# Optimization experiments

Hardware: AMD Instinct MI355X
Metric: run time of the kernel (lower is better)

Reference implementation:

```python
import jax, jax.numpy as jnp
import numpy as np

N_NODES = 100000
N_EDGES = 600000
D = 128
N_CLASSES = 16


def _degrees(idx, n):
    ones = jnp.ones(idx.shape[0], dtype=jnp.float32)
    return jax.ops.segment_sum(ones, idx, num_segments=n)


def graph_conv(src, dst, h, W, b):
    # DGL GraphConv, norm='both': D_out^{-1/2} A D_in^{-1/2} h W + b
    n = h.shape[0]
    deg_out = jnp.maximum(_degrees(src, n), 1.0)
    deg_in = jnp.maximum(_degrees(dst, n), 1.0)
    h = h * jax.lax.rsqrt(deg_out)[:, None]          # src-side norm
    h = h @ W                                         # dense transform
    msg = h[src]                                      # gather  [E, d]
    agg = jax.ops.segment_sum(msg, dst, num_segments=n)  # scatter-add
    agg = agg * jax.lax.rsqrt(deg_in)[:, None]        # dst-side norm
    return agg + b


def setup_inputs() -> dict:
    key = jax.random.key(0)
    ks = jax.random.split(key, 8)
    h = jax.random.normal(ks[0], (N_NODES, D), dtype=jnp.float32)
    src = jax.random.randint(ks[1], (N_EDGES,), 0, N_NODES)
    dst = jax.random.randint(ks[2], (N_EDGES,), 0, N_NODES)
    s = 1.0 / np.sqrt(D)
    W1 = jax.random.normal(ks[3], (D, D), dtype=jnp.float32) * s
    b1 = jnp.zeros((D,), dtype=jnp.float32)
    W2 = jax.random.normal(ks[4], (D, D), dtype=jnp.float32) * s
    b2 = jnp.zeros((D,), dtype=jnp.float32)
    Wc = jax.random.normal(ks[5], (D, N_CLASSES), dtype=jnp.float32) * s
    bc = jnp.zeros((N_CLASSES,), dtype=jnp.float32)
    return {"h": h, "src": src, "dst": dst, "W1": W1, "b1": b1,
            "W2": W2, "b2": b2, "Wc": Wc, "bc": bc}


def reference(h, src, dst, W1, b1, W2, b2, Wc, bc):
    h = jax.nn.relu(graph_conv(src, dst, h, W1, b1))
    h = jax.nn.relu(graph_conv(src, dst, h, W2, b2))
    return h @ Wc + bc
```

## Files before the change

kernel.cpp:

```cpp
#include <hip/hip_runtime.h>


typedef __attribute__((ext_vector_type(4))) _Float16 half4_t;
typedef __attribute__((ext_vector_type(16))) float floatx16;

__global__ __launch_bounds__(256) void scan1_kernel(
    const int* __restrict__ cntI, const int* __restrict__ cntO,
    int* __restrict__ excl, int* __restrict__ bsum,
    float* __restrict__ rs_out, float* __restrict__ rs_in, int n)
{
    __shared__ int tmp[256];
    int i = blockIdx.x * 256 + threadIdx.x;
    int v = 0;
    if (i < n) {
        v = cntI[i];
        rs_in[i]  = rsqrtf(fmaxf((float)v, 1.0f));
        rs_out[i] = rsqrtf(fmaxf((float)cntO[i], 1.0f));
    }
    tmp[threadIdx.x] = v;
    __syncthreads();
    for (int off = 1; off < 256; off <<= 1) {
        int t = (threadIdx.x >= off) ? tmp[threadIdx.x - off] : 0;
        __syncthreads();
        tmp[threadIdx.x] += t;
        __syncthreads();
    }
    if (i < n) excl[i] = tmp[threadIdx.x] - v;
    if (threadIdx.x == 255) bsum[blockIdx.x] = tmp[255];
}

__global__ __launch_bounds__(1024) void scan2_kernel(int* __restrict__ bsum, int nb)
{
    __shared__ int tmp[1024];
    int t = threadIdx.x;
    int v = (t < nb) ? bsum[t] : 0;
    tmp[t] = v;
    __syncthreads();
    for (int off = 1; off < 1024; off <<= 1) {
        int x = (t >= off) ? tmp[t - off] : 0;
        __syncthreads();
        tmp[t] += x;
        __syncthreads();
    }
    if (t < nb) bsum[t] = tmp[t] - v;
}

__global__ __launch_bounds__(256) void scan3_kernel(
    int* __restrict__ excl, const int* __restrict__ bsum, int n)
{
    int i = blockIdx.x * 256 + threadIdx.x;
    if (i < n) excl[i] += bsum[blockIdx.x];
}

__global__ __launch_bounds__(256) void fill_kernel(
    const int* __restrict__ src, const int* __restrict__ dst,
    const int* __restrict__ rank, const int* __restrict__ starts,
    int* __restrict__ eidx, int E)
{
    int e = blockIdx.x * blockDim.x + threadIdx.x;
    if (e < E) {
        eidx[starts[dst[e]] + rank[e]] = src[e];
    }
}

__global__ __launch_bounds__(256) void wpack_kernel(
    const float* __restrict__ W1, const float* __restrict__ W2,
    _Float16* __restrict__ WB1, _Float16* __restrict__ WB2)
{
    int gid = blockIdx.x * 256 + threadIdx.x;
    int j = gid & 16383;
    int i   = j & 3;
    int col = (j >> 2) & 127;
    int g   = (j >> 9) & 1;
    int kt  = j >> 10;
    int k = kt * 8 + g * 4 + i;
    if (gid < 16384) WB1[j] = (_Float16)W1[k * 128 + col];
    else             WB2[j] = (_Float16)W2[k * 128 + col];
}

template <int MODE>
__device__ __forceinline__ void gemm_tile(
    int bid, const void* __restrict__ Xv, const _Float16* __restrict__ WB,
    _Float16* __restrict__ T, int n)
{
    __shared__ _Float16 xa[128 * 128];
    char* xab = (char*)xa;

    const int tid  = threadIdx.x;
    const int lane = tid & 63;
    const int wv   = tid >> 6;
    const int m    = lane & 31;
    const int g    = lane >> 5;
    const int rbase = bid * 128 + wv * 32;

    {
        const int C = (tid & 31) * 4;
        const int rsub = tid >> 5;
#pragma unroll
        for (int p = 0; p < 16; ++p) {
            int R = p * 8 + rsub;
            int row = bid * 128 + R;
            half4_t a;
            if (row < n) {
                if (MODE == 0) {
                    const float* X = (const float*)Xv;
                    float4 v = *(const float4*)&X[(size_t)row * 128 + C];
                    a[0] = (_Float16)v.x;
                    a[1] = (_Float16)v.y;
                    a[2] = (_Float16)v.z;
                    a[3] = (_Float16)v.w;
                } else {
                    const _Float16* X = (const _Float16*)Xv;
                    a = *(const half4_t*)&X[(size_t)row * 128 + C];
                }
            } else {
                a[0] = a[1] = a[2] = a[3] = (_Float16)0.f;
            }
            int byte = (R * 256 + C * 2) ^ ((R & 7) << 4);
            *(half4_t*)(xab + byte) = a;
        }
    }
    __syncthreads();

    floatx16 acc0 = {}, acc1 = {}, acc2 = {}, acc3 = {};
    const int arow = wv * 32 + m;
    const _Float16* wb = WB + (size_t)(g * 128 + m) * 4;

#pragma unroll 2
    for (int kt = 0; kt < 16; ++kt) {
        int cbyte = kt * 16 + g * 8;
        half4_t a = *(const half4_t*)(xab + ((arow * 256 + cbyte) ^ ((m & 7) << 4)));
        const _Float16* wk = wb + (size_t)kt * 1024;
        half4_t b0 = *(const half4_t*)(wk);
        half4_t b1 = *(const half4_t*)(wk + 128);
        half4_t b2 = *(const half4_t*)(wk + 256);
        half4_t b3 = *(const half4_t*)(wk + 384);
        acc0 = __builtin_amdgcn_mfma_f32_32x32x8f16(a, b0, acc0, 0, 0, 0);
        acc1 = __builtin_amdgcn_mfma_f32_32x32x8f16(a, b1, acc1, 0, 0, 0);
        acc2 = __builtin_amdgcn_mfma_f32_32x32x8f16(a, b2, acc2, 0, 0, 0);
        acc3 = __builtin_amdgcn_mfma_f32_32x32x8f16(a, b3, acc3, 0, 0, 0);
    }

#pragma unroll
    for (int rg = 0; rg < 16; ++rg) {
        int rd = (rg & 3) + 8 * (rg >> 2) + 4 * g;
        int orow = rbase + rd;
        if (orow < n) {
            _Float16* tp = T + (size_t)orow * 128 + m;
            tp[0]  = (_Float16)acc0[rg];
            tp[32] = (_Float16)acc1[rg];
            tp[64] = (_Float16)acc2[rg];
            tp[96] = (_Float16)acc3[rg];
        }
    }
}

__global__ __launch_bounds__(256) void fused1_kernel(
    const float* __restrict__ h, const _Float16* __restrict__ WB1,
    _Float16* __restrict__ T1,
    const int* __restrict__ src, const int* __restrict__ dst,
    int* __restrict__ cntO, int* __restrict__ cntI, int* __restrict__ rank,
    int n, int E, int GB, int S)
{
    int bid = blockIdx.x;
    int g = bid / S, r = bid - g * S;
    if (r == 0 && g < GB) {
        gemm_tile<0>(g, h, WB1, T1, n);
    } else {
        int ng = g + (r ? 1 : 0);
        if (ng > GB) ng = GB;
        int cb = bid - ng;
        int t = cb * 256 + threadIdx.x;
        if (t < E) {
            atomicAdd(&cntO[src[t]], 1);
        } else if (t < 2 * E) {
            int e = t - E;
            rank[e] = atomicAdd(&cntI[dst[e]], 1);
        }
    }
}

__global__ __launch_bounds__(256) void gemm2_kernel(
    const _Float16* __restrict__ X, const _Float16* __restrict__ WB,
    _Float16* __restrict__ T, int n)
{
    gemm_tile<1>(blockIdx.x, X, WB, T, n);
}

template <int PES, int NS>
__global__ __launch_bounds__(256) void gather_f16(
    const _Float16* __restrict__ T, const int* __restrict__ eidx,
    const int* __restrict__ starts, const float* __restrict__ rs_in,
    const float* __restrict__ rs_out, const float* __restrict__ bias,
    _Float16* __restrict__ Xout, int n, int E)
{
    int wave = (blockIdx.x * 256 + threadIdx.x) >> 6;
    int lane = threadIdx.x & 63;
    int q = lane >> 5;
    int t = lane & 31;
    int node = wave * 2 + q;
    if (node >= n) return;
    int s0 = starts[node];
    int s1 = (node + 1 < n) ? starts[node + 1] : E;

    float acc[4] = {0.f, 0.f, 0.f, 0.f};
    int j = s0;
    for (; j + 3 < s1; j += 4) {
        int4 s4 = *(const int4*)&eidx[j];
        half4_t va = *(const half4_t*)&T[(size_t)s4.x * 128 + t * 4];
        half4_t vb = *(const half4_t*)&T[(size_t)s4.y * 128 + t * 4];
        half4_t vc = *(const half4_t*)&T[(size_t)s4.z * 128 + t * 4];
        half4_t vd = *(const half4_t*)&T[(size_t)s4.w * 128 + t * 4];
        if (PES) {
            float ra = rs_out[s4.x], rb = rs_out[s4.y];
            float rc = rs_out[s4.z], rd = rs_out[s4.w];
#pragma unroll
            for (int i = 0; i < 4; ++i) {
                acc[i] = fmaf((float)va[i], ra, acc[i]);
                acc[i] = fmaf((float)vb[i], rb, acc[i]);
                acc[i] = fmaf((float)vc[i], rc, acc[i]);
                acc[i] = fmaf((float)vd[i], rd, acc[i]);
            }
        } else {
#pragma unroll
            for (int i = 0; i < 4; ++i)
                acc[i] += ((float)va[i] + (float)vb[i]) + ((float)vc[i] + (float)vd[i]);
        }
    }
    for (; j < s1; ++j) {
        int sA = eidx[j];
        half4_t va = *(const half4_t*)&T[(size_t)sA * 128 + t * 4];
        float ra = PES ? rs_out[sA] : 1.0f;
#pragma unroll
        for (int i = 0; i < 4; ++i) acc[i] = fmaf((float)va[i], ra, acc[i]);
    }

    float ri = rs_in[node];
    float ro = NS ? rs_out[node] : 1.0f;
    float4 bv = *(const float4*)&bias[t * 4];
    float bb[4] = {bv.x, bv.y, bv.z, bv.w};
    half4_t o;
#pragma unroll
    for (int i = 0; i < 4; ++i) {
        float x = fmaxf(fmaf(acc[i], ri, bb[i]), 0.f) * ro;
        o[i] = (_Float16)x;
    }
    *(half4_t*)&Xout[(size_t)node * 128 + t * 4] = o;
}

__global__ __launch_bounds__(256) void classifier_kernel(
    const _Float16* __restrict__ X, const float* __restrict__ Wc,
    const float* __restrict__ bout, float* __restrict__ out, int n)
{
    __shared__ float wl[128 * 16];
    __shared__ _Float16 xs[16][128];
    const int tid = threadIdx.x;
    const int row0 = blockIdx.x * 16;
#pragma unroll
    for (int i0 = 0; i0 < 2; ++i0) {
        int i = tid + i0 * 256;
        ((float4*)wl)[i] = ((const float4*)Wc)[i];
    }
    {
        int r = tid >> 4, c8 = (tid & 15) * 8;
        int row = row0 + r;
        float4 v = make_float4(0.f, 0.f, 0.f, 0.f);
        if (row < n) v = *(const float4*)&X[(size_t)row * 128 + c8];
        *(float4*)&xs[r][c8] = v;
    }
    __syncthreads();
    int c = tid & 15, r = tid >> 4;
    float acc = 0.f;
#pragma unroll 4
    for (int k = 0; k < 128; k += 2) {
        float x0 = (float)xs[r][k];
        float x1 = (float)xs[r][k + 1];
        acc = fmaf(x0, wl[k * 16 + c], acc);
        acc = fmaf(x1, wl[(k + 1) * 16 + c], acc);
    }
    int row = row0 + r;
    if (row < n) out[(size_t)row * 16 + c] = acc + bout[c];
}

extern "C" void kernel_launch(void* const* d_in, const int* in_sizes, int n_in,
                              void* d_out, int out_size, void* d_ws, size_t ws_size,
                              hipStream_t stream)
{
    const float* h   = (const float*)d_in[0];
    const int*   src = (const int*)d_in[1];
    const int*   dst = (const int*)d_in[2];
    const float* W1  = (const float*)d_in[3];
    const float* b1  = (const float*)d_in[4];
    const float* W2  = (const float*)d_in[5];
    const float* b2  = (const float*)d_in[6];
    const float* Wc  = (const float*)d_in[7];
    const float* bc  = (const float*)d_in[8];
    float* out = (float*)d_out;

    const int n = in_sizes[0] / 128;
    const int E = in_sizes[1];
    const int nb = (n + 255) / 256;

    char* ws = (char*)d_ws;
    int*   cntO    = (int*)ws;
    int*   cntI    = cntO + n;
    int*   rank    = cntI + n;
    float* rs_out  = (float*)(rank + E);
    float* rs_in   = rs_out + n;
    int*   starts  = (int*)(rs_in + n);
    int*   bsum    = starts + n;
    int*   eidx    = bsum + 1024;
    _Float16* WB1  = (_Float16*)(eidx + E);
    _Float16* WB2  = WB1 + 16384;
    size_t off = ((size_t)((char*)(WB2 + 16384) - ws) + 255) & ~(size_t)255;
    _Float16* bufA = (_Float16*)(ws + off);
    _Float16* bufB = bufA + (size_t)n * 128;

    const int CB = (2 * E + 255) / 256;
    const int GB = (n + 127) / 128;
    const int S  = (CB + GB) / GB;

    hipMemsetAsync(cntO, 0, (size_t)2 * n * sizeof(int), stream);
    wpack_kernel<<<128, 256, 0, stream>>>(W1, W2, WB1, WB2);
    fused1_kernel<<<CB + GB, 256, 0, stream>>>(h, WB1, bufA, src, dst,
                                               cntO, cntI, rank, n, E, GB, S);
    scan1_kernel<<<nb, 256, 0, stream>>>(cntI, cntO, starts, bsum, rs_out, rs_in, n);
    scan2_kernel<<<1, 1024, 0, stream>>>(bsum, nb);
    scan3_kernel<<<nb, 256, 0, stream>>>(starts, bsum, n);
    fill_kernel<<<(E + 255) / 256, 256, 0, stream>>>(src, dst, rank, starts, eidx, E);

    int ablocks = (n + 7) / 8;

    gather_f16<1, 1><<<ablocks, 256, 0, stream>>>(bufA, eidx, starts, rs_in, rs_out, b1, bufB, n, E);

    gemm2_kernel<<<GB, 256, 0, stream>>>(bufB, WB2, bufA, n);
    gather_f16<0, 0><<<ablocks, 256, 0, stream>>>(bufA, eidx, starts, rs_in, rs_out, b2, bufB, n, E);

    classifier_kernel<<<(n + 15) / 16, 256, 0, stream>>>(bufB, Wc, bc, out, n);
}
```

Before: 202.1 us.

## Fuse classifier into second gather and halve GEMM tile rows

The second-layer gather now applies bias and ReLU and then computes the 128x16 classifier projection in registers, using a 32-lane butterfly shuffle reduction with Wc staged in padded LDS. This removes the classifier kernel launch and the f16 write and re-read of the layer-2 activations. Separately, the GEMM tile shrinks from 128 to 64 rows, with four waves splitting rows and columns, which doubles the block count and halves LDS use. The cost is a per-node 16-way shuffle reduction and a Wc load into LDS in every gather block.

```diff
diff --git a/kernel.cpp b/kernel.cpp
--- a/kernel.cpp
+++ b/kernel.cpp
@@ -79,11 +79,11 @@
 }
 
 template <int MODE>
-__device__ __forceinline__ void gemm_tile(
+__device__ __forceinline__ void gemm_tile64(
     int bid, const void* __restrict__ Xv, const _Float16* __restrict__ WB,
     _Float16* __restrict__ T, int n)
 {
-    __shared__ _Float16 xa[128 * 128];
+    __shared__ _Float16 xa[64 * 128];
     char* xab = (char*)xa;
 
     const int tid  = threadIdx.x;
@@ -91,15 +91,17 @@
     const int wv   = tid >> 6;
     const int m    = lane & 31;
     const int g    = lane >> 5;
-    const int rbase = bid * 128 + wv * 32;
+    const int rhalf = wv & 1;
+    const int chalf = wv >> 1;
+    const int rbase = bid * 64 + rhalf * 32;
 
     {
         const int C = (tid & 31) * 4;
         const int rsub = tid >> 5;
 #pragma unroll
-        for (int p = 0; p < 16; ++p) {
+        for (int p = 0; p < 8; ++p) {
             int R = p * 8 + rsub;
-            int row = bid * 128 + R;
+            int row = bid * 64 + R;
             half4_t a;
             if (row < n) {
                 if (MODE == 0) {
@@ -122,9 +124,9 @@
     }
     __syncthreads();
 
-    floatx16 acc0 = {}, acc1 = {}, acc2 = {}, acc3 = {};
-    const int arow = wv * 32 + m;
-    const _Float16* wb = WB + (size_t)(g * 128 + m) * 4;
+    floatx16 acc0 = {}, acc1 = {};
+    const int arow = rhalf * 32 + m;
+    const _Float16* wb = WB + (size_t)(g * 128 + chalf * 64 + m) * 4;
 
 #pragma unroll 2
     for (int kt = 0; kt < 16; ++kt) {
@@ -133,12 +135,8 @@
         const _Float16* wk = wb + (size_t)kt * 1024;
         half4_t b0 = *(const half4_t*)(wk);
         half4_t b1 = *(const half4_t*)(wk + 128);
-        half4_t b2 = *(const half4_t*)(wk + 256);
-        half4_t b3 = *(const half4_t*)(wk + 384);
         acc0 = __builtin_amdgcn_mfma_f32_32x32x8f16(a, b0, acc0, 0, 0, 0);
         acc1 = __builtin_amdgcn_mfma_f32_32x32x8f16(a, b1, acc1, 0, 0, 0);
-        acc2 = __builtin_amdgcn_mfma_f32_32x32x8f16(a, b2, acc2, 0, 0, 0);
-        acc3 = __builtin_amdgcn_mfma_f32_32x32x8f16(a, b3, acc3, 0, 0, 0);
     }
 
 #pragma unroll
@@ -146,11 +144,9 @@
         int rd = (rg & 3) + 8 * (rg >> 2) + 4 * g;
         int orow = rbase + rd;
         if (orow < n) {
-            _Float16* tp = T + (size_t)orow * 128 + m;
+            _Float16* tp = T + (size_t)orow * 128 + chalf * 64 + m;
             tp[0]  = (_Float16)acc0[rg];
             tp[32] = (_Float16)acc1[rg];
-            tp[64] = (_Float16)acc2[rg];
-            tp[96] = (_Float16)acc3[rg];
         }
     }
 }
@@ -165,7 +161,7 @@
     int bid = blockIdx.x;
     int g = bid / S, r = bid - g * S;
     if (r == 0 && g < GB) {
-        gemm_tile<0>(g, h, WB1, T1, n);
+        gemm_tile64<0>(g, h, WB1, T1, n);
     } else {
         int ng = g + (r ? 1 : 0);
         if (ng > GB) ng = GB;
@@ -184,26 +180,14 @@
     const _Float16* __restrict__ X, const _Float16* __restrict__ WB,
     _Float16* __restrict__ T, int n)
 {
-    gemm_tile<1>(blockIdx.x, X, WB, T, n);
-}
-
-template <int PES, int NS>
-__global__ __launch_bounds__(256) void gather_f16(
+    gemm_tile64<1>(blockIdx.x, X, WB, T, n);
+}
+
+template <int PES>
+__device__ __forceinline__ void edge_accum(
     const _Float16* __restrict__ T, const int* __restrict__ eidx,
-    const int* __restrict__ starts, const float* __restrict__ rs_in,
-    const float* __restrict__ rs_out, const float* __restrict__ bias,
-    _Float16* __restrict__ Xout, int n, int E)
-{
-    int wave = (blockIdx.x * 256 + threadIdx.x) >> 6;
-    int lane = threadIdx.x & 63;
-    int q = lane >> 5;
-    int t = lane & 31;
-    int node = wave * 2 + q;
-    if (node >= n) return;
-    int s0 = starts[node];
-    int s1 = (node + 1 < n) ? starts[node + 1] : E;
-
-    float acc[4] = {0.f, 0.f, 0.f, 0.f};
+    const float* __restrict__ rs_out, int s0, int s1, int t, float acc[4])
+{
     int j = s0;
     for (; j + 3 < s1; j += 4) {
         int4 s4 = *(const int4*)&eidx[j];
@@ -234,9 +218,28 @@
 #pragma unroll
         for (int i = 0; i < 4; ++i) acc[i] = fmaf((float)va[i], ra, acc[i]);
     }
+}
+
+__global__ __launch_bounds__(256) void gather1_kernel(
+    const _Float16* __restrict__ T, const int* __restrict__ eidx,
+    const int* __restrict__ starts, const float* __restrict__ rs_in,
+    const float* __restrict__ rs_out, const float* __restrict__ bias,
+    _Float16* __restrict__ Xout, int n, int E)
+{
+    int wave = (blockIdx.x * 256 + threadIdx.x) >> 6;
+    int lane = threadIdx.x & 63;
+    int q = lane >> 5;
+    int t = lane & 31;
+    int node = wave * 2 + q;
+    if (node >= n) return;
+    int s0 = starts[node];
+    int s1 = (node + 1 < n) ? starts[node + 1] : E;
+
+    float acc[4] = {0.f, 0.f, 0.f, 0.f};
+    edge_accum<1>(T, eidx, rs_out, s0, s1, t, acc);
 
     float ri = rs_in[node];
-    float ro = NS ? rs_out[node] : 1.0f;
+    float ro = rs_out[node];
     float4 bv = *(const float4*)&bias[t * 4];
     float bb[4] = {bv.x, bv.y, bv.z, bv.w};
     half4_t o;
@@ -248,38 +251,62 @@
     *(half4_t*)&Xout[(size_t)node * 128 + t * 4] = o;
 }
 
-__global__ __launch_bounds__(256) void classifier_kernel(
-    const _Float16* __restrict__ X, const float* __restrict__ Wc,
-    const float* __restrict__ bout, float* __restrict__ out, int n)
-{
-    __shared__ float wl[128 * 16];
-    __shared__ _Float16 xs[16][128];
-    const int tid = threadIdx.x;
-    const int row0 = blockIdx.x * 16;
-#pragma unroll
-    for (int i0 = 0; i0 < 2; ++i0) {
-        int i = tid + i0 * 256;
-        ((float4*)wl)[i] = ((const float4*)Wc)[i];
-    }
-    {
-        int r = tid >> 4, c8 = (tid & 15) * 8;
-        int row = row0 + r;
-        float4 v = make_float4(0.f, 0.f, 0.f, 0.f);
-        if (row < n) v = *(const float4*)&X[(size_t)row * 128 + c8];
-        *(float4*)&xs[r][c8] = v;
+__global__ __launch_bounds__(256) void gather2cls_kernel(
+    const _Float16* __restrict__ T, const int* __restrict__ eidx,
+    const int* __restrict__ starts, const float* __restrict__ rs_in,
+    const float* __restrict__ bias, const float* __restrict__ Wc,
+    const float* __restrict__ bc_, float* __restrict__ outp, int n, int E)
+{
+    __shared__ float wcl[128 * 17];
+    for (int j = threadIdx.x; j < 2048; j += 256) {
+        int k = j >> 4, c = j & 15;
+        wcl[k * 17 + c] = Wc[j];
     }
     __syncthreads();
-    int c = tid & 15, r = tid >> 4;
-    float acc = 0.f;
-#pragma unroll 4
-    for (int k = 0; k < 128; k += 2) {
-        float x0 = (float)xs[r][k];
-        float x1 = (float)xs[r][k + 1];
-        acc = fmaf(x0, wl[k * 16 + c], acc);
-        acc = fmaf(x1, wl[(k + 1) * 16 + c], acc);
-    }
-    int row = row0 + r;
-    if (row < n) out[(size_t)row * 16 + c] = acc + bout[c];
+
+    int wave = (blockIdx.x * 256 + threadIdx.x) >> 6;
+    int lane = threadIdx.x & 63;
+    int q = lane >> 5;
+    int t = lane & 31;
+    int node = wave * 2 + q;
+    if (node >= n) return;
+    int s0 = starts[node];
+    int s1 = (node + 1 < n) ? starts[node + 1] : E;
+
+    float acc[4] = {0.f, 0.f, 0.f, 0.f};
+    edge_accum<0>(T, eidx, nullptr, s0, s1, t, acc);
+
+    float ri = rs_in[node];
+    float4 bv = *(const float4*)&bias[t * 4];
+    float bb[4] = {bv.x, bv.y, bv.z, bv.w};
+    float x[4];
+#pragma unroll
+    for (int i = 0; i < 4; ++i)
+        x[i] = fmaxf(fmaf(acc[i], ri, bb[i]), 0.f);
+
+    float loc[16];
+#pragma unroll
+    for (int c = 0; c < 16; ++c) loc[c] = 0.f;
+#pragma unroll
+    for (int i = 0; i < 4; ++i) {
+        int k = t * 4 + i;
+#pragma unroll
+        for (int c = 0; c < 16; ++c)
+            loc[c] = fmaf(x[i], wcl[k * 17 + c], loc[c]);
+    }
+#pragma unroll
+    for (int step = 1; step < 32; step <<= 1) {
+#pragma unroll
+        for (int c = 0; c < 16; ++c)
+            loc[c] += __shfl_xor(loc[c], step, 32);
+    }
+    if (t < 16) {
+        float v = loc[0];
+#pragma unroll
+        for (int c = 1; c < 16; ++c)
+            if (t == c) v = loc[c];
+        outp[(size_t)node * 16 + t] = v + bc_[t];
+    }
 }
 
 extern "C" void kernel_launch(void* const* d_in, const int* in_sizes, int n_in,
@@ -317,7 +344,7 @@
     _Float16* bufB = bufA + (size_t)n * 128;
 
     const int CB = (2 * E + 255) / 256;
-    const int GB = (n + 127) / 128;
+    const int GB = (n + 63) / 64;
     const int S  = (CB + GB) / GB;
 
     hipMemsetAsync(cntO, 0, (size_t)2 * n * sizeof(int), stream);
@@ -331,10 +358,9 @@
 
     int ablocks = (n + 7) / 8;
 
-    gather_f16<1, 1><<<ablocks, 256, 0, stream>>>(bufA, eidx, starts, rs_in, rs_out, b1, bufB, n, E);
+    gather1_kernel<<<ablocks, 256, 0, stream>>>(bufA, eidx, starts, rs_in, rs_out, b1, bufB, n, E);
 
     gemm2_kernel<<<GB, 256, 0, stream>>>(bufB, WB2, bufA, n);
-    gather_f16<0, 0><<<ablocks, 256, 0, stream>>>(bufA, eidx, starts, rs_in, rs_out, b2, bufB, n, E);
-
-    classifier_kernel<<<(n + 15) / 16, 256, 0, stream>>>(bufB, Wc, bc, out, n);
-}
+
+    gather2cls_kernel<<<ablocks, 256, 0, stream>>>(bufA, eidx, starts, rs_in, b2, Wc, bc, out, n, E);
+}
```

Result: slower. 218.2 us (+8.0%).
